# Kernel optimization log

Measured on AMD Instinct MI355X. Metric: run time of the kernel, lower is better.

Reference implementation:

```python
import jax, jax.numpy as jnp
import numpy as np

B, S, D = 2, 2048, 1024
H = 16
HD = D // H  # 64
SCALE = 1.0 / np.sqrt(HD)


def setup_inputs() -> dict:
    key = jax.random.key(0)
    k1, k2, k3, k4, k5 = jax.random.split(key, 5)
    std = 0.02
    return {
        "Q_input": jax.random.normal(k1, (B, S, D), dtype=jnp.float32),
        "Wq": jax.random.normal(k2, (D, H * HD), dtype=jnp.float32) * std,
        "Wk": jax.random.normal(k3, (D, HD), dtype=jnp.float32) * std,
        "Wv": jax.random.normal(k4, (D, HD), dtype=jnp.float32) * std,
        "Wo": jax.random.normal(k5, (H * HD, D), dtype=jnp.float32) * std,
    }


def reference(Q_input, Wq, Wk, Wv, Wo):
    b, s, _ = Q_input.shape
    # projections; K/V use a single shared head (MQA)
    Q = (Q_input @ Wq).reshape(b, s, H, HD)   # [b,s,H,hd]
    K = Q_input @ Wk                           # [b,s,hd]
    V = Q_input @ Wv                           # [b,s,hd]
    # scores: broadcast the single KV head across all H query heads
    scores = jnp.einsum("bqhd,bkd->bhqk", Q, K) * SCALE  # [b,H,s,s]
    probs = jax.nn.softmax(scores, axis=-1)
    ctx = jnp.einsum("bhqk,bkd->bqhd", probs, V)          # [b,s,H,hd]
    out = ctx.reshape(b, s, H * HD) @ Wo                  # [b,s,D]
    return out
```

## Files before the change

### kernel.cpp

```cpp
#include <hip/hip_runtime.h>

typedef __attribute__((ext_vector_type(8))) short bf16x8;
typedef __attribute__((ext_vector_type(4))) float f32x4;
typedef __attribute__((ext_vector_type(4))) unsigned int u32x4;
typedef unsigned short u16;

#define MFMA16(a,b,c) __builtin_amdgcn_mfma_f32_16x16x32_bf16((a),(b),(c),0,0,0)

__device__ __forceinline__ u16 f2bf(float f){
  unsigned int u = __float_as_uint(f);
  u += 0x7fffu + ((u >> 16) & 1u);
  return (u16)(u >> 16);
}
__device__ __forceinline__ float bf2f(u16 v){
  return __uint_as_float(((unsigned int)v) << 16);
}
__device__ __forceinline__ unsigned int cvtpk(float lo, float hi){
  unsigned int r;
  asm("v_cvt_pk_bf16_f32 %0, %1, %2" : "=v"(r) : "v"(lo), "v"(hi));
  return r;
}
__device__ __forceinline__ void gload16(const void* g, void* l){
  __builtin_amdgcn_global_load_lds(
      (__attribute__((address_space(1))) void*)g,
      (__attribute__((address_space(3))) void*)l, 16, 0, 0);
}

__global__ __launch_bounds__(256) void mqa_cvt(const float* __restrict__ in,
                                               u16* __restrict__ out, int n8){
  int i = blockIdx.x * 256 + threadIdx.x;
  if (i >= n8) return;
  const float4* p = (const float4*)in;
  float4 a = p[2*i], b = p[2*i+1];
  u16 o[8] = { f2bf(a.x), f2bf(a.y), f2bf(a.z), f2bf(a.w),
               f2bf(b.x), f2bf(b.y), f2bf(b.z), f2bf(b.w) };
  *(bf16x8*)&out[(size_t)i*8] = *(bf16x8*)o;
}

__global__ __launch_bounds__(256) void mqa_tcvt4(
    const float* __restrict__ Wq, const float* __restrict__ Wk,
    const float* __restrict__ Wv, const float* __restrict__ Wo,
    u16* __restrict__ WT, u16* __restrict__ WoT)
{
  __shared__ float t[32][33];
  int bx = blockIdx.x;
  const float* src; u16* dst; int C, cb, rb;
  if (bx < 1024)      { src = Wq; dst = WT;                      C = 1024; int q = bx;        cb = q & 31; rb = q >> 5; }
  else if (bx < 1088) { src = Wk; dst = WT + (size_t)1024*1024;  C = 64;   int q = bx - 1024; cb = q & 1;  rb = q >> 1; }
  else if (bx < 1152) { src = Wv; dst = WT + (size_t)1088*1024;  C = 64;   int q = bx - 1088; cb = q & 1;  rb = q >> 1; }
  else                { src = Wo; dst = WoT;                     C = 1024; int q = bx - 1152; cb = q & 31; rb = q >> 5; }
  int c0 = cb * 32, r0 = rb * 32;
  int x = threadIdx.x & 31, y0 = threadIdx.x >> 5;
  #pragma unroll
  for (int yy = y0; yy < 32; yy += 8)
    t[yy][x] = src[(size_t)(r0 + yy) * C + c0 + x];
  __syncthreads();
  #pragma unroll
  for (int yy = y0; yy < 32; yy += 8)
    dst[(size_t)(c0 + yy) * 1024 + r0 + x] = f2bf(t[x][yy]);
}

template<int EPI>
__global__ __launch_bounds__(256, 3) void mqa_gemm(
    const u16* __restrict__ A, const u16* __restrict__ Bt,
    float* __restrict__ outF, u16* __restrict__ Qb, u16* __restrict__ Kb,
    u16* __restrict__ Vtb, int M, int N, int K, int NT)
{
  __shared__ __align__(16) u16 lds_a[2][64*64];
  __shared__ __align__(16) u16 lds_b[2][128*64];
  int bx = blockIdx.x;
  int mt = bx / NT, nt = bx % NT;
  int m0 = mt * 64, n0 = nt * 128;
  int tid = threadIdx.x;
  int wid = tid >> 6, lane = tid & 63;
  int wr = (wid >> 1) * 32, wc = (wid & 1) * 64;
  int srow = lane >> 3;
  int scol = ((lane & 7) ^ srow) * 8;
  int fr = lane & 15, g = lane >> 4, fg = lane >> 4;
  int sw = fr & 7;

  f32x4 acc[2][4];
  #pragma unroll
  for (int i = 0; i < 2; ++i)
    #pragma unroll
    for (int j = 0; j < 4; ++j) acc[i][j] = (f32x4)0.f;

  auto stage = [&](int bi, int k0){
    #pragma unroll
    for (int cc = 0; cc < 3; ++cc) {
      int c = 3*wid + cc;
      #pragma unroll
      for (int j = 0; j < 2; ++j) {
        if (c < 4) {
          int row = c*16 + j*8;
          gload16(&A [(size_t)(m0 + row + srow) * K + k0 + scol], &lds_a[bi][row*64]);
        } else {
          int row = (c-4)*16 + j*8;
          gload16(&Bt[(size_t)(n0 + row + srow) * K + k0 + scol], &lds_b[bi][row*64]);
        }
      }
    }
  };

  stage(0, 0);
  __syncthreads();
  int cur = 0;
  for (int k0 = 0; k0 < K; k0 += 64) {
    if (k0 + 64 < K) stage(cur ^ 1, k0 + 64);
    #pragma unroll
    for (int ks = 0; ks < 2; ++ks) {
      bf16x8 af[2], bfr[4];
      #pragma unroll
      for (int i = 0; i < 2; ++i)
        af[i] = *(const bf16x8*)&lds_a[cur][(wr + i*16 + fr)*64 + (((ks*4+g) ^ sw))*8];
      #pragma unroll
      for (int j = 0; j < 4; ++j)
        bfr[j] = *(const bf16x8*)&lds_b[cur][(wc + j*16 + fr)*64 + (((ks*4+g) ^ sw))*8];
      #pragma unroll
      for (int i = 0; i < 2; ++i)
        #pragma unroll
        for (int j = 0; j < 4; ++j)
          acc[i][j] = MFMA16(af[i], bfr[j], acc[i][j]);
    }
    __syncthreads();
    cur ^= 1;
  }

  #pragma unroll
  for (int i = 0; i < 2; ++i) {
    #pragma unroll
    for (int j = 0; j < 4; ++j) {
      int ncol = n0 + wc + j*16 + fr;
      #pragma unroll
      for (int r = 0; r < 4; ++r) {
        int m = m0 + wr + i*16 + fg*4 + r;
        float v = acc[i][j][r];
        if (EPI == 0) {
          outF[(size_t)m * N + ncol] = v;
        } else {
          u16 bv = f2bf(v);
          if (ncol < 1024) {
            Qb[(size_t)m * 1024 + ncol] = bv;
          } else if (ncol < 1088) {
            Kb[(size_t)m * 64 + (ncol - 1024)] = bv;
          } else {
            int b = m >> 11, s = m & 2047;
            int k = s & 63;
            int pos = (k & 35) | ((k & 12) << 1) | ((k & 16) >> 2);
            Vtb[((size_t)b * 64 + (ncol - 1088)) * 2048 + (s & ~63) + pos] = bv;
          }
        }
      }
    }
  }
}

__global__ __launch_bounds__(256, 4) void mqa_attn(
    const u16* __restrict__ Qb, const u16* __restrict__ Kb,
    const u16* __restrict__ Vtb, u16* __restrict__ Opart,
    float* __restrict__ Lpart)
{
  const float C1 = 0.18033688011112042f;
  const float MC = 32.f * C1;
  int qt = blockIdx.x, h = blockIdx.y;
  int b = blockIdx.z >> 1, sp = blockIdx.z & 1;
  int part = blockIdx.z;
  int tid = threadIdx.x, wid = tid >> 6, lane = tid & 63;
  int fr = lane & 15, g = lane >> 4;
  int q0 = qt * 128 + wid * 32;

  __shared__ __align__(16) u16 KT[2][64*64];
  __shared__ __align__(16) u16 VT[2][64*64];

  const u16* Qbase = Qb + (size_t)b * 2048 * 1024 + (size_t)h * 64;
  const u16* Kbase = Kb + (size_t)b * 2048 * 64;
  const u16* Vbase = Vtb + (size_t)b * 64 * 2048;

  int srow = lane >> 3;
  int scol = ((lane & 7) ^ srow) * 8;

  bf16x8 qfv[2][2];
  #pragma unroll
  for (int qf_ = 0; qf_ < 2; ++qf_)
    #pragma unroll
    for (int ks = 0; ks < 2; ++ks)
      qfv[qf_][ks] = *(const bf16x8*)&Qbase[(size_t)(q0 + qf_*16 + fr) * 1024 + ks*32 + g*8];

  f32x4 oacc[2][4];
  #pragma unroll
  for (int qf_ = 0; qf_ < 2; ++qf_)
    #pragma unroll
    for (int vf = 0; vf < 4; ++vf) oacc[qf_][vf] = (f32x4)0.f;
  float lacc0 = 0.f, lacc1 = 0.f;

  const int kb0 = sp * 16;

  #pragma unroll
  for (int j = 0; j < 2; ++j) {
    int row = wid*16 + j*8 + srow;
    gload16(&Kbase[(size_t)(kb0*64 + row) * 64 + scol], &KT[0][(wid*16 + j*8) * 64]);
    gload16(&Vbase[(size_t)row * 2048 + kb0*64 + scol], &VT[0][(wid*16 + j*8) * 64]);
  }
  __syncthreads();

  int cur = 0;
  for (int kb = kb0; kb < kb0 + 16; ++kb) {
    int ntl = (kb + 1 < kb0 + 16) ? kb + 1 : kb0;
    #pragma unroll
    for (int j = 0; j < 2; ++j) {
      int row = wid*16 + j*8 + srow;
      gload16(&Kbase[(size_t)(ntl*64 + row) * 64 + scol], &KT[cur^1][(wid*16 + j*8) * 64]);
      gload16(&Vbase[(size_t)row * 2048 + ntl*64 + scol], &VT[cur^1][(wid*16 + j*8) * 64]);
    }

    const u16* kc = &KT[cur][0];
    const u16* vc = &VT[cur][0];

    f32x4 sacc[2][4];
    #pragma unroll
    for (int qf_ = 0; qf_ < 2; ++qf_)
      #pragma unroll
      for (int kf = 0; kf < 4; ++kf) sacc[qf_][kf] = (f32x4)0.f;

    __builtin_amdgcn_s_setprio(1);
    #pragma unroll
    for (int ks = 0; ks < 2; ++ks) {
      #pragma unroll
      for (int kf = 0; kf < 4; ++kf) {
        bf16x8 kfr = *(const bf16x8*)&kc[(kf*16 + fr)*64 + (((ks*4+g) ^ (fr&7)))*8];
        sacc[0][kf] = MFMA16(kfr, qfv[0][ks], sacc[0][kf]);
        sacc[1][kf] = MFMA16(kfr, qfv[1][ks], sacc[1][kf]);
      }
    }
    __builtin_amdgcn_s_setprio(0);

    unsigned int pk0[8], pk1[8];
    float s0 = 0.f, s1 = 0.f;
    #pragma unroll
    for (int kf = 0; kf < 4; ++kf) {
      float a0 = __builtin_amdgcn_exp2f(sacc[0][kf][0] * C1 - MC);
      float a1 = __builtin_amdgcn_exp2f(sacc[0][kf][1] * C1 - MC);
      float a2 = __builtin_amdgcn_exp2f(sacc[0][kf][2] * C1 - MC);
      float a3 = __builtin_amdgcn_exp2f(sacc[0][kf][3] * C1 - MC);
      s0 += (a0 + a1) + (a2 + a3);
      pk0[2*kf]   = cvtpk(a0, a1);
      pk0[2*kf+1] = cvtpk(a2, a3);
      float b0 = __builtin_amdgcn_exp2f(sacc[1][kf][0] * C1 - MC);
      float b1 = __builtin_amdgcn_exp2f(sacc[1][kf][1] * C1 - MC);
      float b2 = __builtin_amdgcn_exp2f(sacc[1][kf][2] * C1 - MC);
      float b3 = __builtin_amdgcn_exp2f(sacc[1][kf][3] * C1 - MC);
      s1 += (b0 + b1) + (b2 + b3);
      pk1[2*kf]   = cvtpk(b0, b1);
      pk1[2*kf+1] = cvtpk(b2, b3);
    }
    lacc0 += s0;
    lacc1 += s1;

    __builtin_amdgcn_s_setprio(1);
    #pragma unroll
    for (int ks2 = 0; ks2 < 2; ++ks2) {
      u32x4 w0 = { pk0[4*ks2], pk0[4*ks2+1], pk0[4*ks2+2], pk0[4*ks2+3] };
      u32x4 w1 = { pk1[4*ks2], pk1[4*ks2+1], pk1[4*ks2+2], pk1[4*ks2+3] };
      bf16x8 pA0 = __builtin_bit_cast(bf16x8, w0);
      bf16x8 pA1 = __builtin_bit_cast(bf16x8, w1);
      #pragma unroll
      for (int vf = 0; vf < 4; ++vf) {
        bf16x8 vfr = *(const bf16x8*)&vc[(vf*16 + fr)*64 + (((ks2*4+g) ^ (fr&7)))*8];
        oacc[0][vf] = MFMA16(pA0, vfr, oacc[0][vf]);
        oacc[1][vf] = MFMA16(pA1, vfr, oacc[1][vf]);
      }
    }
    __builtin_amdgcn_s_setprio(0);

    __syncthreads();
    cur ^= 1;
  }

  lacc0 += __shfl_xor(lacc0, 16); lacc0 += __shfl_xor(lacc0, 32);
  lacc1 += __shfl_xor(lacc1, 16); lacc1 += __shfl_xor(lacc1, 32);

  #pragma unroll
  for (int qf_ = 0; qf_ < 2; ++qf_) {
    #pragma unroll
    for (int r = 0; r < 4; ++r) {
      int row = q0 + qf_*16 + g*4 + r;
      #pragma unroll
      for (int vf = 0; vf < 4; ++vf) {
        int col = h*64 + vf*16 + fr;
        Opart[((size_t)part * 2048 + row) * 1024 + col] = f2bf(oacc[qf_][vf][r]);
      }
    }
  }
  if (g == 0) {
    int q = q0 + fr;
    size_t base = ((size_t)part * 16 + h) * 2048;
    Lpart[base + q]      = lacc0;
    Lpart[base + q + 16] = lacc1;
  }
}

__global__ __launch_bounds__(256) void mqa_merge(
    const u16* __restrict__ Opart, const float* __restrict__ Lpart,
    u16* __restrict__ Ctx)
{
  int idx = blockIdx.x * 256 + threadIdx.x;
  int cg  = idx & 255;
  int row = (idx >> 8) & 2047;
  int b   = idx >> 19;
  int h   = cg >> 4;
  size_t mb0 = ((size_t)(b*2 + 0) * 16 + h) * 2048 + row;
  size_t mb1 = ((size_t)(b*2 + 1) * 16 + h) * 2048 + row;
  float rl = 1.f / (Lpart[mb0] + Lpart[mb1]);
  size_t o0 = ((size_t)(b*2 + 0) * 2048 + row) * 1024 + cg * 4;
  size_t o1 = ((size_t)(b*2 + 1) * 2048 + row) * 1024 + cg * 4;
  ushort4 a = *(const ushort4*)&Opart[o0];
  ushort4 c = *(const ushort4*)&Opart[o1];
  u16 o[4];
  o[0] = f2bf((bf2f(a.x) + bf2f(c.x)) * rl);
  o[1] = f2bf((bf2f(a.y) + bf2f(c.y)) * rl);
  o[2] = f2bf((bf2f(a.z) + bf2f(c.z)) * rl);
  o[3] = f2bf((bf2f(a.w) + bf2f(c.w)) * rl);
  *(ushort4*)&Ctx[((size_t)b * 2048 + row) * 1024 + cg * 4] = *(ushort4*)o;
}

extern "C" void kernel_launch(void* const* d_in, const int* in_sizes, int n_in,
                              void* d_out, int out_size, void* d_ws, size_t ws_size,
                              hipStream_t stream)
{
  const float* Qin = (const float*)d_in[0];
  const float* Wq  = (const float*)d_in[1];
  const float* Wk  = (const float*)d_in[2];
  const float* Wv  = (const float*)d_in[3];
  const float* Wo  = (const float*)d_in[4];
  float* out = (float*)d_out;

  u16* Xb  = (u16*)d_ws;
  u16* WT  = Xb  + (size_t)4096*1024;
  u16* WoT = WT  + (size_t)1152*1024;
  u16* Qb  = WoT + (size_t)1024*1024;
  u16* Kb  = Qb  + (size_t)4096*1024;
  u16* Vtb = Kb  + (size_t)4096*64;
  u16* Ctx = Vtb + (size_t)2*64*2048;
  float* Lpart = (float*)(Ctx + (size_t)4096*1024);

  u16* Opart = (u16*)d_out;

  mqa_cvt<<<2048, 256, 0, stream>>>(Qin, Xb, 4096*1024/8);
  mqa_tcvt4<<<2176, 256, 0, stream>>>(Wq, Wk, Wv, Wo, WT, WoT);

  mqa_gemm<1><<<64*9, 256, 0, stream>>>(Xb, WT, nullptr, Qb, Kb, Vtb,
                                        4096, 1152, 1024, 9);
  mqa_attn<<<dim3(16,16,4), 256, 0, stream>>>(Qb, Kb, Vtb, Opart, Lpart);
  mqa_merge<<<4096, 256, 0, stream>>>(Opart, Lpart, Ctx);
  mqa_gemm<0><<<64*8, 256, 0, stream>>>(Ctx, WoT, out, nullptr, nullptr, nullptr,
                                        4096, 1024, 1024, 8);
}
```

Baseline: 101.7 us.

## Fuse input conversion and split-KV merge into GEMM A-tile loads

Removes the standalone fp32-to-bf16 conversion kernel and the split-KV merge kernel. The QKV GEMM now reads fp32 input directly and packs it to bf16 while staging into LDS. The output GEMM reads the two partial outputs and their normalizers, combines them on the fly, and writes the result into LDS. This saves two launches and the intermediate bf16 buffers. In exchange, A-tile staging moves from async global-to-LDS loads to register loads plus ALU work, which could reduce overlap. Other changes: workgroup index remapping across groups of 8, reusing the WT region for Opart, and skipping the redundant wraparound prefetch in attention.

Result: no change. 102.6 us (+0.9%).

```diff
diff --git a/kernel.cpp b/kernel.cpp
--- a/kernel.cpp
+++ b/kernel.cpp
@@ -24,17 +24,6 @@
   __builtin_amdgcn_global_load_lds(
       (__attribute__((address_space(1))) void*)g,
       (__attribute__((address_space(3))) void*)l, 16, 0, 0);
-}
-
-__global__ __launch_bounds__(256) void mqa_cvt(const float* __restrict__ in,
-                                               u16* __restrict__ out, int n8){
-  int i = blockIdx.x * 256 + threadIdx.x;
-  if (i >= n8) return;
-  const float4* p = (const float4*)in;
-  float4 a = p[2*i], b = p[2*i+1];
-  u16 o[8] = { f2bf(a.x), f2bf(a.y), f2bf(a.z), f2bf(a.w),
-               f2bf(b.x), f2bf(b.y), f2bf(b.z), f2bf(b.w) };
-  *(bf16x8*)&out[(size_t)i*8] = *(bf16x8*)o;
 }
 
 __global__ __launch_bounds__(256) void mqa_tcvt4(
@@ -60,24 +49,31 @@
     dst[(size_t)(c0 + yy) * 1024 + r0 + x] = f2bf(t[x][yy]);
 }
 
-template<int EPI>
+template<int MODE>
 __global__ __launch_bounds__(256, 3) void mqa_gemm(
-    const u16* __restrict__ A, const u16* __restrict__ Bt,
+    const float* __restrict__ Af, const u16* __restrict__ Op,
+    const float* __restrict__ Lp, const u16* __restrict__ Bt,
     float* __restrict__ outF, u16* __restrict__ Qb, u16* __restrict__ Kb,
     u16* __restrict__ Vtb, int M, int N, int K, int NT)
 {
   __shared__ __align__(16) u16 lds_a[2][64*64];
   __shared__ __align__(16) u16 lds_b[2][128*64];
-  int bx = blockIdx.x;
+  int nwg = gridDim.x;
+  int bx = ((int)blockIdx.x & 7) * (nwg >> 3) + ((int)blockIdx.x >> 3);
   int mt = bx / NT, nt = bx % NT;
   int m0 = mt * 64, n0 = nt * 128;
   int tid = threadIdx.x;
   int wid = tid >> 6, lane = tid & 63;
   int wr = (wid >> 1) * 32, wc = (wid & 1) * 64;
+  int fr = lane & 15, g = lane >> 4;
+  int sw = fr & 7;
+
+  int ar = tid >> 2, ac = (tid & 3) * 16;
+  int m_a = m0 + ar;
+  int ab = m_a >> 11, as_ = m_a & 2047;
+  int c8a = ac >> 3, rw8 = ar & 7;
   int srow = lane >> 3;
   int scol = ((lane & 7) ^ srow) * 8;
-  int fr = lane & 15, g = lane >> 4, fg = lane >> 4;
-  int sw = fr & 7;
 
   f32x4 acc[2][4];
   #pragma unroll
@@ -85,28 +81,70 @@
     #pragma unroll
     for (int j = 0; j < 4; ++j) acc[i][j] = (f32x4)0.f;
 
-  auto stage = [&](int bi, int k0){
-    #pragma unroll
-    for (int cc = 0; cc < 3; ++cc) {
-      int c = 3*wid + cc;
-      #pragma unroll
-      for (int j = 0; j < 2; ++j) {
-        if (c < 4) {
-          int row = c*16 + j*8;
-          gload16(&A [(size_t)(m0 + row + srow) * K + k0 + scol], &lds_a[bi][row*64]);
-        } else {
-          int row = (c-4)*16 + j*8;
-          gload16(&Bt[(size_t)(n0 + row + srow) * K + k0 + scol], &lds_b[bi][row*64]);
-        }
-      }
+  float4 fA[4];
+  bf16x8 pA0, pA1, pB0, pB1;
+  float rlA = 0.f;
+
+  auto loadA = [&](int k0){
+    if (MODE == 1) {
+      const float* src = &Af[(size_t)m_a * K + k0 + ac];
+      fA[0] = *(const float4*)(src);
+      fA[1] = *(const float4*)(src + 4);
+      fA[2] = *(const float4*)(src + 8);
+      fA[3] = *(const float4*)(src + 12);
+    } else {
+      int h = k0 >> 6;
+      float l0 = Lp[(((size_t)(ab*2    ))*16 + h)*2048 + as_];
+      float l1 = Lp[(((size_t)(ab*2 + 1))*16 + h)*2048 + as_];
+      rlA = 1.f / (l0 + l1);
+      const u16* p0 = &Op[(((size_t)(ab*2    ))*2048 + as_)*1024 + k0 + ac];
+      const u16* p1 = &Op[(((size_t)(ab*2 + 1))*2048 + as_)*1024 + k0 + ac];
+      pA0 = *(const bf16x8*)p0; pA1 = *(const bf16x8*)(p0 + 8);
+      pB0 = *(const bf16x8*)p1; pB1 = *(const bf16x8*)(p1 + 8);
     }
   };
 
-  stage(0, 0);
+  auto writeA = [&](int bi){
+    unsigned int w0[4], w1[4];
+    if (MODE == 1) {
+      w0[0] = cvtpk(fA[0].x, fA[0].y); w0[1] = cvtpk(fA[0].z, fA[0].w);
+      w0[2] = cvtpk(fA[1].x, fA[1].y); w0[3] = cvtpk(fA[1].z, fA[1].w);
+      w1[0] = cvtpk(fA[2].x, fA[2].y); w1[1] = cvtpk(fA[2].z, fA[2].w);
+      w1[2] = cvtpk(fA[3].x, fA[3].y); w1[3] = cvtpk(fA[3].z, fA[3].w);
+    } else {
+      #pragma unroll
+      for (int j = 0; j < 4; ++j) {
+        float e0 = (bf2f((u16)pA0[2*j  ]) + bf2f((u16)pB0[2*j  ])) * rlA;
+        float e1 = (bf2f((u16)pA0[2*j+1]) + bf2f((u16)pB0[2*j+1])) * rlA;
+        w0[j] = cvtpk(e0, e1);
+        float e2 = (bf2f((u16)pA1[2*j  ]) + bf2f((u16)pB1[2*j  ])) * rlA;
+        float e3 = (bf2f((u16)pA1[2*j+1]) + bf2f((u16)pB1[2*j+1])) * rlA;
+        w1[j] = cvtpk(e2, e3);
+      }
+    }
+    u32x4 v0 = { w0[0], w0[1], w0[2], w0[3] };
+    u32x4 v1 = { w1[0], w1[1], w1[2], w1[3] };
+    *(bf16x8*)&lds_a[bi][ar*64 + ((c8a    ) ^ rw8)*8] = __builtin_bit_cast(bf16x8, v0);
+    *(bf16x8*)&lds_a[bi][ar*64 + ((c8a + 1) ^ rw8)*8] = __builtin_bit_cast(bf16x8, v1);
+  };
+
+  auto stageB = [&](int bi, int k0){
+    #pragma unroll
+    for (int cc = 0; cc < 4; ++cc) {
+      int rb = (wid*4 + cc) * 8;
+      gload16(&Bt[(size_t)(n0 + rb + srow) * K + k0 + scol], &lds_b[bi][rb*64]);
+    }
+  };
+
+  loadA(0);
+  stageB(0, 0);
+  writeA(0);
   __syncthreads();
+
   int cur = 0;
   for (int k0 = 0; k0 < K; k0 += 64) {
-    if (k0 + 64 < K) stage(cur ^ 1, k0 + 64);
+    bool nx = (k0 + 64 < K);
+    if (nx) { loadA(k0 + 64); stageB(cur ^ 1, k0 + 64); }
     #pragma unroll
     for (int ks = 0; ks < 2; ++ks) {
       bf16x8 af[2], bfr[4];
@@ -122,10 +160,12 @@
         for (int j = 0; j < 4; ++j)
           acc[i][j] = MFMA16(af[i], bfr[j], acc[i][j]);
     }
+    if (nx) writeA(cur ^ 1);
     __syncthreads();
     cur ^= 1;
   }
 
+  int fg = g;
   #pragma unroll
   for (int i = 0; i < 2; ++i) {
     #pragma unroll
@@ -135,7 +175,7 @@
       for (int r = 0; r < 4; ++r) {
         int m = m0 + wr + i*16 + fg*4 + r;
         float v = acc[i][j][r];
-        if (EPI == 0) {
+        if (MODE == 2) {
           outF[(size_t)m * N + ncol] = v;
         } else {
           u16 bv = f2bf(v);
@@ -205,12 +245,14 @@
 
   int cur = 0;
   for (int kb = kb0; kb < kb0 + 16; ++kb) {
-    int ntl = (kb + 1 < kb0 + 16) ? kb + 1 : kb0;
-    #pragma unroll
-    for (int j = 0; j < 2; ++j) {
-      int row = wid*16 + j*8 + srow;
-      gload16(&Kbase[(size_t)(ntl*64 + row) * 64 + scol], &KT[cur^1][(wid*16 + j*8) * 64]);
-      gload16(&Vbase[(size_t)row * 2048 + ntl*64 + scol], &VT[cur^1][(wid*16 + j*8) * 64]);
+    if (kb + 1 < kb0 + 16) {
+      int ntl = kb + 1;
+      #pragma unroll
+      for (int j = 0; j < 2; ++j) {
+        int row = wid*16 + j*8 + srow;
+        gload16(&Kbase[(size_t)(ntl*64 + row) * 64 + scol], &KT[cur^1][(wid*16 + j*8) * 64]);
+        gload16(&Vbase[(size_t)row * 2048 + ntl*64 + scol], &VT[cur^1][(wid*16 + j*8) * 64]);
+      }
     }
 
     const u16* kc = &KT[cur][0];
@@ -299,30 +341,6 @@
   }
 }
 
-__global__ __launch_bounds__(256) void mqa_merge(
-    const u16* __restrict__ Opart, const float* __restrict__ Lpart,
-    u16* __restrict__ Ctx)
-{
-  int idx = blockIdx.x * 256 + threadIdx.x;
-  int cg  = idx & 255;
-  int row = (idx >> 8) & 2047;
-  int b   = idx >> 19;
-  int h   = cg >> 4;
-  size_t mb0 = ((size_t)(b*2 + 0) * 16 + h) * 2048 + row;
-  size_t mb1 = ((size_t)(b*2 + 1) * 16 + h) * 2048 + row;
-  float rl = 1.f / (Lpart[mb0] + Lpart[mb1]);
-  size_t o0 = ((size_t)(b*2 + 0) * 2048 + row) * 1024 + cg * 4;
-  size_t o1 = ((size_t)(b*2 + 1) * 2048 + row) * 1024 + cg * 4;
-  ushort4 a = *(const ushort4*)&Opart[o0];
-  ushort4 c = *(const ushort4*)&Opart[o1];
-  u16 o[4];
-  o[0] = f2bf((bf2f(a.x) + bf2f(c.x)) * rl);
-  o[1] = f2bf((bf2f(a.y) + bf2f(c.y)) * rl);
-  o[2] = f2bf((bf2f(a.z) + bf2f(c.z)) * rl);
-  o[3] = f2bf((bf2f(a.w) + bf2f(c.w)) * rl);
-  *(ushort4*)&Ctx[((size_t)b * 2048 + row) * 1024 + cg * 4] = *(ushort4*)o;
-}
-
 extern "C" void kernel_launch(void* const* d_in, const int* in_sizes, int n_in,
                               void* d_out, int out_size, void* d_ws, size_t ws_size,
                               hipStream_t stream)
@@ -334,24 +352,21 @@
   const float* Wo  = (const float*)d_in[4];
   float* out = (float*)d_out;
 
-  u16* Xb  = (u16*)d_ws;
-  u16* WT  = Xb  + (size_t)4096*1024;
-  u16* WoT = WT  + (size_t)1152*1024;
+  u16* WoT = (u16*)d_ws;
   u16* Qb  = WoT + (size_t)1024*1024;
   u16* Kb  = Qb  + (size_t)4096*1024;
   u16* Vtb = Kb  + (size_t)4096*64;
-  u16* Ctx = Vtb + (size_t)2*64*2048;
-  float* Lpart = (float*)(Ctx + (size_t)4096*1024);
-
-  u16* Opart = (u16*)d_out;
-
-  mqa_cvt<<<2048, 256, 0, stream>>>(Qin, Xb, 4096*1024/8);
+  float* Lpart = (float*)(Vtb + (size_t)2*64*2048);
+  u16* WT    = (u16*)(Lpart + (size_t)4*16*2048);
+  u16* Opart = WT;
+
   mqa_tcvt4<<<2176, 256, 0, stream>>>(Wq, Wk, Wv, Wo, WT, WoT);
 
-  mqa_gemm<1><<<64*9, 256, 0, stream>>>(Xb, WT, nullptr, Qb, Kb, Vtb,
+  mqa_gemm<1><<<64*9, 256, 0, stream>>>(Qin, nullptr, nullptr, WT,
+                                        nullptr, Qb, Kb, Vtb,
                                         4096, 1152, 1024, 9);
   mqa_attn<<<dim3(16,16,4), 256, 0, stream>>>(Qb, Kb, Vtb, Opart, Lpart);
-  mqa_merge<<<4096, 256, 0, stream>>>(Opart, Lpart, Ctx);
-  mqa_gemm<0><<<64*8, 256, 0, stream>>>(Ctx, WoT, out, nullptr, nullptr, nullptr,
+  mqa_gemm<2><<<64*8, 256, 0, stream>>>(nullptr, Opart, Lpart, WoT,
+                                        out, nullptr, nullptr, nullptr,
                                         4096, 1024, 1024, 8);
 }
```
